# Performance work log

Measured on AMD Instinct MI355X. Metric: run time of the kernel, lower is better.

Reference implementation:

```python
import jax, jax.numpy as jnp
import numpy as np
from jax import lax

B, F, N, C = 1024, 256, 65536, 1000
SOURCE_CLASSES = 751
TEMP = 0.05
MOMENTUM = 0.2


def setup_inputs() -> dict:
    key = jax.random.key(0)
    k1, k2, k3, k4 = jax.random.split(key, 4)
    inputs = jax.random.normal(k1, (B, F), dtype=jnp.float32)
    # indexes in [1, N] so that (indexes - 1) are all valid -> the boolean mask
    # `inds = indexes >= 0` keeps every row (static shapes under jit)
    indexes = jax.random.randint(k2, (B,), 1, N + 1, dtype=jnp.int32)
    features = jax.random.normal(k3, (N, F), dtype=jnp.float32)
    features = features / jnp.linalg.norm(features, axis=1, keepdims=True)  # bank stores unit rows
    labels = jax.random.randint(k4, (N,), 0, C, dtype=jnp.int32)
    return {"inputs": inputs, "indexes": indexes, "features": features, "labels": labels}


def _forward(inputs, idx, features, labels):
    # F.normalize(inputs, dim=1)
    x = inputs / jnp.linalg.norm(inputs, axis=1, keepdims=True)           # [B, F]
    logits = (x @ features.T) / TEMP                                      # [B, N]
    targets = labels[idx]                                                 # [B]
    # sim.index_add_(0, labels, inputs.t()) -> per-class column sums
    sim = jax.ops.segment_sum(logits.T, labels, num_segments=C)           # [C, B]
    nums = jax.ops.segment_sum(jnp.ones((N,), jnp.float32), labels, num_segments=C)  # [C]
    mask = nums > 0
    sim = sim / jnp.where(mask, nums, 1.0)[:, None]                       # per-class mean
    # masked softmax over classes (faithful to original: plain exp, +eps denominator)
    exps = jnp.exp(sim.T) * mask[None, :].astype(jnp.float32)            # [B, C]
    p = exps / (exps.sum(axis=1, keepdims=True) + 1e-6)
    logp = jnp.log(p + 1e-6)
    # F.nll_loss(..., ignore_index=source_classes-1)
    valid = (targets != SOURCE_CLASSES - 1).astype(jnp.float32)
    nll = -jnp.take_along_axis(logp, targets[:, None], axis=1)[:, 0]
    loss = jnp.sum(nll * valid) / jnp.maximum(valid.sum(), 1.0)
    return loss, x


def reference(inputs, indexes, features, labels):
    idx = indexes - 1
    idx = jnp.where(idx == 5554, SOURCE_CLASSES - 1, idx)  # is_source=True special case
    loss, x = _forward(inputs, idx, features, labels)
    # HM.backward's per-sample sequential momentum scatter update + renorm of the bank.
    # Order-dependent on duplicate indices -> inherently sequential -> lax.scan.
    def step(feats, xy):
        xi, yi = xy
        row = MOMENTUM * feats[yi] + (1.0 - MOMENTUM) * xi
        row = row / jnp.linalg.norm(row)
        return feats.at[yi].set(row), None

    new_features, _ = lax.scan(step, features, (x, idx))
    return loss, new_features
```

## Files before the change

### kernel.cpp

```cpp
#include <hip/hip_runtime.h>
#include <math.h>

#define Bn   1024
#define Fdim 256
#define Nn   65536
#define Cn   1000
#define INV_TEMP 20.0f
#define MOM  0.2f

struct WS {
  float x[Bn * Fdim];
  float meanT[Fdim * Cn];
  float mask[Cn];
  float sumExp[Bn];
  float tExp[Bn];
  int   idx[Bn];
  int   targets[Bn];
  int   counts[Cn];
  int   offsets[Cn];
  int   cursor[Cn];
  int   list[Nn];
};

__global__ void k0_zero(int* __restrict__ counts, float* __restrict__ sumExp) {
  int t = blockIdx.x * blockDim.x + threadIdx.x;
  if (t < Cn) counts[t] = 0;
  if (t < Bn) sumExp[t] = 0.f;
}

__global__ void k1_norm(const float* __restrict__ inputs, const int* __restrict__ indexes,
                        const int* __restrict__ labels, float* __restrict__ x,
                        int* __restrict__ idx, int* __restrict__ targets) {
  int b = blockIdx.x, t = threadIdx.x;
  float v = inputs[b * Fdim + t];
  float s = v * v;
#pragma unroll
  for (int o = 32; o > 0; o >>= 1) s += __shfl_down(s, o, 64);
  __shared__ float red[4];
  if ((t & 63) == 0) red[t >> 6] = s;
  __syncthreads();
  float tot = red[0] + red[1] + red[2] + red[3];
  float inv = 1.0f / sqrtf(tot);
  x[b * Fdim + t] = v * inv;
  if (t == 0) {
    int i0 = indexes[b] - 1;
    if (i0 == 5554) i0 = 750;
    idx[b] = i0;
    targets[b] = labels[i0];
  }
}

__global__ void k2_count(const int* __restrict__ labels, int* __restrict__ counts) {
  int n = blockIdx.x * blockDim.x + threadIdx.x;
  atomicAdd(&counts[labels[n]], 1);
}

__global__ void k3_scan(const int* __restrict__ counts, int* __restrict__ offsets,
                        int* __restrict__ cursor) {
  __shared__ int s[1024];
  int t = threadIdx.x;
  int v = (t < Cn) ? counts[t] : 0;
  s[t] = v;
  __syncthreads();
  for (int o = 1; o < 1024; o <<= 1) {
    int a = (t >= o) ? s[t - o] : 0;
    __syncthreads();
    s[t] += a;
    __syncthreads();
  }
  if (t < Cn) {
    int off = s[t] - v;
    offsets[t] = off;
    cursor[t] = off;
  }
}

__global__ void k4_fill(const int* __restrict__ labels, int* __restrict__ cursor,
                        int* __restrict__ list) {
  int n = blockIdx.x * blockDim.x + threadIdx.x;
  int c = labels[n];
  int p = atomicAdd(&cursor[c], 1);
  list[p] = n;
}

__global__ void k5_classsum(const float* __restrict__ features, const int* __restrict__ list,
                            const int* __restrict__ offsets, const int* __restrict__ counts,
                            float* __restrict__ meanT, float* __restrict__ mask,
                            float* __restrict__ out1) {
  int c = blockIdx.x, t = threadIdx.x;
  int off = offsets[c], cnt = counts[c];
  __shared__ int mlds[256];
  float acc = 0.f;
  for (int base = 0; base < cnt; base += 256) {
    int m = min(256, cnt - base);
    if (t < m) mlds[t] = list[off + base + t];
    __syncthreads();
    int i = 0;
    for (; i + 4 <= m; i += 4) {
      int n0 = mlds[i], n1 = mlds[i + 1], n2 = mlds[i + 2], n3 = mlds[i + 3];
      float v0 = features[n0 * Fdim + t];
      float v1 = features[n1 * Fdim + t];
      float v2 = features[n2 * Fdim + t];
      float v3 = features[n3 * Fdim + t];
      acc += v0 + v1 + v2 + v3;
      out1[n0 * Fdim + t] = v0;
      out1[n1 * Fdim + t] = v1;
      out1[n2 * Fdim + t] = v2;
      out1[n3 * Fdim + t] = v3;
    }
    for (; i < m; i++) {
      int n = mlds[i];
      float v = features[n * Fdim + t];
      acc += v;
      out1[n * Fdim + t] = v;
    }
    __syncthreads();
  }
  meanT[t * Cn + c] = (cnt > 0) ? acc / (float)cnt : 0.f;
  if (t == 0) mask[c] = (cnt > 0) ? 1.f : 0.f;
}

#define BBT 8
__global__ void k6_matmul(const float* __restrict__ x, const float* __restrict__ meanT,
                          const float* __restrict__ mask, const int* __restrict__ targets,
                          float* __restrict__ sumExp, float* __restrict__ tExp) {
  int b0 = blockIdx.x * BBT, c0 = blockIdx.y * 256;
  int t = threadIdx.x;
  __shared__ float xs[BBT][Fdim];
#pragma unroll
  for (int bb = 0; bb < BBT; bb++) xs[bb][t] = x[(b0 + bb) * Fdim + t];
  __syncthreads();
  int c = c0 + t;
  bool cv = (c < Cn);
  float acc[BBT];
#pragma unroll
  for (int bb = 0; bb < BBT; bb++) acc[bb] = 0.f;
  for (int f = 0; f < Fdim; f += 4) {
    float mv0 = cv ? meanT[(f + 0) * Cn + c] : 0.f;
    float mv1 = cv ? meanT[(f + 1) * Cn + c] : 0.f;
    float mv2 = cv ? meanT[(f + 2) * Cn + c] : 0.f;
    float mv3 = cv ? meanT[(f + 3) * Cn + c] : 0.f;
#pragma unroll
    for (int bb = 0; bb < BBT; bb++) {
      float4 xv = *(const float4*)&xs[bb][f];
      acc[bb] += xv.x * mv0 + xv.y * mv1 + xv.z * mv2 + xv.w * mv3;
    }
  }
  float msk = cv ? mask[c] : 0.f;
  __shared__ float red[4];
#pragma unroll 1
  for (int bb = 0; bb < BBT; bb++) {
    float e = msk * expf(acc[bb] * INV_TEMP);
    float s = e;
#pragma unroll
    for (int o = 32; o > 0; o >>= 1) s += __shfl_down(s, o, 64);
    if ((t & 63) == 0) red[t >> 6] = s;
    __syncthreads();
    if (t == 0) atomicAdd(&sumExp[b0 + bb], red[0] + red[1] + red[2] + red[3]);
    int tgt = targets[b0 + bb];
    if (cv && tgt == c) tExp[b0 + bb] = e;
    __syncthreads();
  }
}

__global__ void k7_loss(const float* __restrict__ sumExp, const float* __restrict__ tExp,
                        const int* __restrict__ targets, float* __restrict__ out) {
  int t = threadIdx.x;
  float S = sumExp[t], tE = tExp[t];
  float nll = -logf(tE / (S + 1e-6f) + 1e-6f);
  float valid = (targets[t] != 750) ? 1.f : 0.f;
  float a = nll * valid, b = valid;
#pragma unroll
  for (int o = 32; o > 0; o >>= 1) {
    a += __shfl_down(a, o, 64);
    b += __shfl_down(b, o, 64);
  }
  __shared__ float ra[16], rb[16];
  if ((t & 63) == 0) { ra[t >> 6] = a; rb[t >> 6] = b; }
  __syncthreads();
  if (t == 0) {
    float sa = 0.f, sb = 0.f;
    for (int i = 0; i < 16; i++) { sa += ra[i]; sb += rb[i]; }
    out[0] = sa / fmaxf(sb, 1.f);
  }
}

__global__ __launch_bounds__(256) void k8_update(const float* __restrict__ features,
                                                 const float* __restrict__ x,
                                                 const int* __restrict__ idx,
                                                 float* __restrict__ out1) {
  __shared__ int ilds[Bn];
  int t = threadIdx.x;
  for (int i = t; i < Bn; i += 256) ilds[i] = idx[i];
  __syncthreads();
  int wid = t >> 6, lane = t & 63;
  int b = blockIdx.x * 4 + wid;
  int y = ilds[b];
  for (int base = 0; base < b; base += 64) {
    int j = base + lane;
    bool hit = (j < b) && (ilds[j] == y);
    if (__any(hit)) return;
  }
  float4 r = *(const float4*)&features[y * Fdim + lane * 4];
  for (int base = (b >> 6) << 6; base < Bn; base += 64) {
    int k = base + lane;
    bool hit = (k >= b) && (ilds[k] == y);
    unsigned long long mbits = __ballot(hit);
    while (mbits) {
      int p = __ffsll(mbits) - 1;
      mbits &= mbits - 1;
      int kk = base + p;
      float4 xv = *(const float4*)&x[kk * Fdim + lane * 4];
      r.x = MOM * r.x + (1.f - MOM) * xv.x;
      r.y = MOM * r.y + (1.f - MOM) * xv.y;
      r.z = MOM * r.z + (1.f - MOM) * xv.z;
      r.w = MOM * r.w + (1.f - MOM) * xv.w;
      float ss = r.x * r.x + r.y * r.y + r.z * r.z + r.w * r.w;
#pragma unroll
      for (int o = 32; o > 0; o >>= 1) ss += __shfl_xor(ss, o, 64);
      float inv = 1.0f / sqrtf(ss);
      r.x *= inv; r.y *= inv; r.z *= inv; r.w *= inv;
    }
  }
  int base2 = y * Fdim + lane * 4;
  out1[base2 + 0] = r.x;
  out1[base2 + 1] = r.y;
  out1[base2 + 2] = r.z;
  out1[base2 + 3] = r.w;
}

extern "C" void kernel_launch(void* const* d_in, const int* in_sizes, int n_in,
                              void* d_out, int out_size, void* d_ws, size_t ws_size,
                              hipStream_t stream) {
  const float* inputs   = (const float*)d_in[0];
  const int*   indexes  = (const int*)d_in[1];
  const float* features = (const float*)d_in[2];
  const int*   labels   = (const int*)d_in[3];
  float* out = (float*)d_out;
  WS* w = (WS*)d_ws;

  k0_zero<<<4, 256, 0, stream>>>(w->counts, w->sumExp);
  k1_norm<<<Bn, 256, 0, stream>>>(inputs, indexes, labels, w->x, w->idx, w->targets);
  k2_count<<<Nn / 256, 256, 0, stream>>>(labels, w->counts);
  k3_scan<<<1, 1024, 0, stream>>>(w->counts, w->offsets, w->cursor);
  k4_fill<<<Nn / 256, 256, 0, stream>>>(labels, w->cursor, w->list);
  k5_classsum<<<Cn, 256, 0, stream>>>(features, w->list, w->offsets, w->counts,
                                      w->meanT, w->mask, out + 1);
  k6_matmul<<<dim3(Bn / BBT, 4), 256, 0, stream>>>(w->x, w->meanT, w->mask, w->targets,
                                                   w->sumExp, w->tExp);
  k7_loss<<<1, 1024, 0, stream>>>(w->sumExp, w->tExp, w->targets, out);
  k8_update<<<Bn / 4, 256, 0, stream>>>(features, w->x, w->idx, out + 1);
}
```

Before: 219.7 us.

## Vectorize class-sum and matmul with packed float4 layout and wave-level reductions

The class-sum kernel now uses 512 threads with eight waves, each reading whole feature rows as float4. It reduces partial sums through shared memory and writes the class means in a packed float4-interleaved layout. The matmul reads that layout with one float4 load per four features, takes x directly from global memory instead of LDS, and replaces the block-level barrier reduction with per-wave atomics and fast exp. The norm kernel shrinks to one wave per row with float4 loads. These changes target memory-access efficiency and barrier overhead, at the cost of more atomics on sumExp.

```diff
diff --git a/kernel.cpp b/kernel.cpp
--- a/kernel.cpp
+++ b/kernel.cpp
@@ -10,7 +10,7 @@
 
 struct WS {
   float x[Bn * Fdim];
-  float meanT[Fdim * Cn];
+  float meanP[Fdim * Cn];
   float mask[Cn];
   float sumExp[Bn];
   float tExp[Bn];
@@ -28,20 +28,19 @@
   if (t < Bn) sumExp[t] = 0.f;
 }
 
-__global__ void k1_norm(const float* __restrict__ inputs, const int* __restrict__ indexes,
-                        const int* __restrict__ labels, float* __restrict__ x,
-                        int* __restrict__ idx, int* __restrict__ targets) {
+__global__ __launch_bounds__(64) void k1_norm(const float* __restrict__ inputs,
+                                              const int* __restrict__ indexes,
+                                              const int* __restrict__ labels,
+                                              float* __restrict__ x,
+                                              int* __restrict__ idx, int* __restrict__ targets) {
   int b = blockIdx.x, t = threadIdx.x;
-  float v = inputs[b * Fdim + t];
-  float s = v * v;
-#pragma unroll
-  for (int o = 32; o > 0; o >>= 1) s += __shfl_down(s, o, 64);
-  __shared__ float red[4];
-  if ((t & 63) == 0) red[t >> 6] = s;
-  __syncthreads();
-  float tot = red[0] + red[1] + red[2] + red[3];
-  float inv = 1.0f / sqrtf(tot);
-  x[b * Fdim + t] = v * inv;
+  float4 v = *(const float4*)&inputs[b * Fdim + t * 4];
+  float s = v.x * v.x + v.y * v.y + v.z * v.z + v.w * v.w;
+#pragma unroll
+  for (int o = 32; o > 0; o >>= 1) s += __shfl_xor(s, o, 64);
+  float inv = 1.0f / sqrtf(s);
+  v.x *= inv; v.y *= inv; v.z *= inv; v.w *= inv;
+  *(float4*)&x[b * Fdim + t * 4] = v;
   if (t == 0) {
     int i0 = indexes[b] - 1;
     if (i0 == 5554) i0 = 750;
@@ -83,83 +82,92 @@
   list[p] = n;
 }
 
-__global__ void k5_classsum(const float* __restrict__ features, const int* __restrict__ list,
-                            const int* __restrict__ offsets, const int* __restrict__ counts,
-                            float* __restrict__ meanT, float* __restrict__ mask,
-                            float* __restrict__ out1) {
-  int c = blockIdx.x, t = threadIdx.x;
+__global__ __launch_bounds__(512) void k5_classsum(const float* __restrict__ features,
+                                                   const int* __restrict__ list,
+                                                   const int* __restrict__ offsets,
+                                                   const int* __restrict__ counts,
+                                                   float* __restrict__ meanP,
+                                                   float* __restrict__ mask,
+                                                   float* __restrict__ out1) {
+  int c = blockIdx.x, t = threadIdx.x, w = t >> 6, lane = t & 63;
   int off = offsets[c], cnt = counts[c];
-  __shared__ int mlds[256];
-  float acc = 0.f;
-  for (int base = 0; base < cnt; base += 256) {
-    int m = min(256, cnt - base);
+  __shared__ int mlds[512];
+  __shared__ float partial[8][256];
+  float4 acc = {0.f, 0.f, 0.f, 0.f};
+  for (int base = 0; base < cnt; base += 512) {
+    int m = min(512, cnt - base);
     if (t < m) mlds[t] = list[off + base + t];
     __syncthreads();
-    int i = 0;
-    for (; i + 4 <= m; i += 4) {
-      int n0 = mlds[i], n1 = mlds[i + 1], n2 = mlds[i + 2], n3 = mlds[i + 3];
-      float v0 = features[n0 * Fdim + t];
-      float v1 = features[n1 * Fdim + t];
-      float v2 = features[n2 * Fdim + t];
-      float v3 = features[n3 * Fdim + t];
-      acc += v0 + v1 + v2 + v3;
-      out1[n0 * Fdim + t] = v0;
-      out1[n1 * Fdim + t] = v1;
-      out1[n2 * Fdim + t] = v2;
-      out1[n3 * Fdim + t] = v3;
-    }
-    for (; i < m; i++) {
+    int i = w;
+    for (; i + 8 < m; i += 16) {
+      int n0 = mlds[i], n1 = mlds[i + 8];
+      float4 v0 = *(const float4*)&features[n0 * Fdim + lane * 4];
+      float4 v1 = *(const float4*)&features[n1 * Fdim + lane * 4];
+      acc.x += v0.x + v1.x; acc.y += v0.y + v1.y;
+      acc.z += v0.z + v1.z; acc.w += v0.w + v1.w;
+      float* o0 = &out1[n0 * Fdim + lane * 4];
+      o0[0] = v0.x; o0[1] = v0.y; o0[2] = v0.z; o0[3] = v0.w;
+      float* o1 = &out1[n1 * Fdim + lane * 4];
+      o1[0] = v1.x; o1[1] = v1.y; o1[2] = v1.z; o1[3] = v1.w;
+    }
+    for (; i < m; i += 8) {
       int n = mlds[i];
-      float v = features[n * Fdim + t];
-      acc += v;
-      out1[n * Fdim + t] = v;
-    }
-    __syncthreads();
-  }
-  meanT[t * Cn + c] = (cnt > 0) ? acc / (float)cnt : 0.f;
-  if (t == 0) mask[c] = (cnt > 0) ? 1.f : 0.f;
+      float4 v = *(const float4*)&features[n * Fdim + lane * 4];
+      acc.x += v.x; acc.y += v.y; acc.z += v.z; acc.w += v.w;
+      float* o = &out1[n * Fdim + lane * 4];
+      o[0] = v.x; o[1] = v.y; o[2] = v.z; o[3] = v.w;
+    }
+    __syncthreads();
+  }
+  *(float4*)&partial[w][lane * 4] = acc;
+  __syncthreads();
+  if (t < 256) {
+    float s = 0.f;
+#pragma unroll
+    for (int ww = 0; ww < 8; ww++) s += partial[ww][t];
+    meanP[((t >> 2) * Cn + c) * 4 + (t & 3)] = (cnt > 0) ? s / (float)cnt : 0.f;
+    if (t == 0) mask[c] = (cnt > 0) ? 1.f : 0.f;
+  }
 }
 
 #define BBT 8
-__global__ void k6_matmul(const float* __restrict__ x, const float* __restrict__ meanT,
-                          const float* __restrict__ mask, const int* __restrict__ targets,
-                          float* __restrict__ sumExp, float* __restrict__ tExp) {
-  int b0 = blockIdx.x * BBT, c0 = blockIdx.y * 256;
-  int t = threadIdx.x;
-  __shared__ float xs[BBT][Fdim];
-#pragma unroll
-  for (int bb = 0; bb < BBT; bb++) xs[bb][t] = x[(b0 + bb) * Fdim + t];
-  __syncthreads();
-  int c = c0 + t;
+__global__ __launch_bounds__(256) void k6_matmul(const float* __restrict__ x,
+                                                 const float* __restrict__ meanP,
+                                                 const float* __restrict__ mask,
+                                                 const int* __restrict__ targets,
+                                                 float* __restrict__ sumExp,
+                                                 float* __restrict__ tExp) {
+  int b0 = blockIdx.x * BBT;
+  int c  = blockIdx.y * 256 + threadIdx.x;
+  int lane = threadIdx.x & 63;
   bool cv = (c < Cn);
+  int cc = cv ? c : 0;
   float acc[BBT];
 #pragma unroll
   for (int bb = 0; bb < BBT; bb++) acc[bb] = 0.f;
-  for (int f = 0; f < Fdim; f += 4) {
-    float mv0 = cv ? meanT[(f + 0) * Cn + c] : 0.f;
-    float mv1 = cv ? meanT[(f + 1) * Cn + c] : 0.f;
-    float mv2 = cv ? meanT[(f + 2) * Cn + c] : 0.f;
-    float mv3 = cv ? meanT[(f + 3) * Cn + c] : 0.f;
+  const float* xb = x + b0 * Fdim;
+#pragma unroll 4
+  for (int f4 = 0; f4 < Fdim / 4; f4++) {
+    float4 mv = *(const float4*)&meanP[(f4 * Cn + cc) * 4];
 #pragma unroll
     for (int bb = 0; bb < BBT; bb++) {
-      float4 xv = *(const float4*)&xs[bb][f];
-      acc[bb] += xv.x * mv0 + xv.y * mv1 + xv.z * mv2 + xv.w * mv3;
-    }
-  }
-  float msk = cv ? mask[c] : 0.f;
-  __shared__ float red[4];
-#pragma unroll 1
+      float4 xv = *(const float4*)&xb[bb * Fdim + f4 * 4];
+      acc[bb] = fmaf(xv.x, mv.x, acc[bb]);
+      acc[bb] = fmaf(xv.y, mv.y, acc[bb]);
+      acc[bb] = fmaf(xv.z, mv.z, acc[bb]);
+      acc[bb] = fmaf(xv.w, mv.w, acc[bb]);
+    }
+  }
+  float msk = cv ? mask[cc] : 0.f;
+#pragma unroll
   for (int bb = 0; bb < BBT; bb++) {
-    float e = msk * expf(acc[bb] * INV_TEMP);
+    float e = msk * __expf(acc[bb] * INV_TEMP);
     float s = e;
 #pragma unroll
     for (int o = 32; o > 0; o >>= 1) s += __shfl_down(s, o, 64);
-    if ((t & 63) == 0) red[t >> 6] = s;
-    __syncthreads();
-    if (t == 0) atomicAdd(&sumExp[b0 + bb], red[0] + red[1] + red[2] + red[3]);
+    if (lane == 0) atomicAdd(&sumExp[b0 + bb], s);
     int tgt = targets[b0 + bb];
     if (cv && tgt == c) tExp[b0 + bb] = e;
-    __syncthreads();
   }
 }
 
@@ -240,13 +248,13 @@
   WS* w = (WS*)d_ws;
 
   k0_zero<<<4, 256, 0, stream>>>(w->counts, w->sumExp);
-  k1_norm<<<Bn, 256, 0, stream>>>(inputs, indexes, labels, w->x, w->idx, w->targets);
+  k1_norm<<<Bn, 64, 0, stream>>>(inputs, indexes, labels, w->x, w->idx, w->targets);
   k2_count<<<Nn / 256, 256, 0, stream>>>(labels, w->counts);
   k3_scan<<<1, 1024, 0, stream>>>(w->counts, w->offsets, w->cursor);
   k4_fill<<<Nn / 256, 256, 0, stream>>>(labels, w->cursor, w->list);
-  k5_classsum<<<Cn, 256, 0, stream>>>(features, w->list, w->offsets, w->counts,
-                                      w->meanT, w->mask, out + 1);
-  k6_matmul<<<dim3(Bn / BBT, 4), 256, 0, stream>>>(w->x, w->meanT, w->mask, w->targets,
+  k5_classsum<<<Cn, 512, 0, stream>>>(features, w->list, w->offsets, w->counts,
+                                      w->meanP, w->mask, out + 1);
+  k6_matmul<<<dim3(Bn / BBT, 4), 256, 0, stream>>>(w->x, w->meanP, w->mask, w->targets,
                                                    w->sumExp, w->tExp);
   k7_loss<<<1, 1024, 0, stream>>>(w->sumExp, w->tExp, w->targets, out);
   k8_update<<<Bn / 4, 256, 0, stream>>>(features, w->x, w->idx, out + 1);
```

Result: faster. 213.6 us (-2.8%).
